# Kernel optimization log

Hardware: AMD Instinct MI355X
Metric: run time of the kernel (lower is better)

The kernel has to match this reference:

```python
import jax, jax.numpy as jnp
import numpy as np

N_IN, N_HID, HEADS = 7, 28, 7
HEAD_DIM = N_HID // HEADS  # 4
LN_EPS = 1e-5


def setup_inputs() -> dict:
    key = jax.random.key(0)
    ks = jax.random.split(key, 16)
    B, S = 16, 1024
    s_in = 1.0 / np.sqrt(N_IN)
    s_hid = 1.0 / np.sqrt(N_HID)
    inp = {
        "inputs": jax.random.normal(ks[0], (B, S, N_IN), dtype=jnp.float32),
        "Wq": jax.random.normal(ks[1], (N_IN, N_HID), dtype=jnp.float32) * s_in,
        "bq": jax.random.normal(ks[2], (N_HID,), dtype=jnp.float32) * s_in,
        "Wk": jax.random.normal(ks[3], (N_IN, N_HID), dtype=jnp.float32) * s_in,
        "bk": jax.random.normal(ks[4], (N_HID,), dtype=jnp.float32) * s_in,
        "Wv": jax.random.normal(ks[5], (N_IN, N_HID), dtype=jnp.float32) * s_in,
        "bv": jax.random.normal(ks[6], (N_HID,), dtype=jnp.float32) * s_in,
        "ln_w": jnp.ones((N_HID,), dtype=jnp.float32),
        "ln_b": jnp.zeros((N_HID,), dtype=jnp.float32),
        "W1": jax.random.normal(ks[7], (N_HID, N_IN), dtype=jnp.float32) * s_hid,
        "b1": jax.random.normal(ks[8], (N_IN,), dtype=jnp.float32) * s_hid,
        "Wq2": jax.random.normal(ks[9], (N_IN, N_HID), dtype=jnp.float32) * s_in,
        "bq2": jax.random.normal(ks[10], (N_HID,), dtype=jnp.float32) * s_in,
        "Wk2": jax.random.normal(ks[11], (N_IN, N_HID), dtype=jnp.float32) * s_in,
        "bk2": jax.random.normal(ks[12], (N_HID,), dtype=jnp.float32) * s_in,
    }
    return inp


def reference(inputs, Wq, bq, Wk, bk, Wv, bv, ln_w, ln_b, W1, b1, Wq2, bq2, Wk2, bk2):
    B, S, _ = inputs.shape
    # QKV projections -> [B, S, H, Dh]
    Q = (inputs @ Wq + bq).reshape(B, S, HEADS, HEAD_DIM)
    K = (inputs @ Wk + bk).reshape(B, S, HEADS, HEAD_DIM)
    V = (inputs @ Wv + bv).reshape(B, S, HEADS, HEAD_DIM)
    # multi-head attention, scores [B, H, Sq, Sk]
    scores = jnp.einsum("bqhd,bkhd->bhqk", Q, K) / jnp.sqrt(jnp.float32(HEAD_DIM))
    attn = jax.nn.softmax(scores, axis=-1)
    out = jnp.einsum("bhqk,bkhd->bqhd", attn, V).reshape(B, S, N_HID)
    # LayerNorm over last dim
    mu = jnp.mean(out, axis=-1, keepdims=True)
    var = jnp.var(out, axis=-1, keepdims=True)
    out = (out - mu) / jnp.sqrt(var + LN_EPS) * ln_w + ln_b
    # FFN + relu + residual
    out = jax.nn.relu(out @ W1 + b1) + inputs  # [B, S, N_IN]
    # second attention (weights only)
    Q2 = out @ Wq2 + bq2  # [B, S, N_HID]
    K2 = out @ Wk2 + bk2
    scores2 = jnp.einsum("bqh,bkh->bqk", Q2, K2) / jnp.sqrt(jnp.float32(N_IN))
    attn2 = jax.nn.softmax(scores2, axis=-1)  # [B, S, S]
    return (out, attn2)
```

## Files before the change

kernel.cpp:

```cpp
#include <hip/hip_runtime.h>

#define BB 16
#define SS 1024
#define NIN 7
#define NHID 28
#define NH 7
#define DH 4

#define EXP2F(x) __builtin_amdgcn_exp2f(x)

constexpr int ROWS = BB * SS;
constexpr int QKV_ELEMS = BB * NH * SS * DH;
constexpr int CHUNK_STRIDE = BB * NH * SS;

__global__ __launch_bounds__(256) void k_proj(
    const float* __restrict__ inp,
    const float* __restrict__ Wq, const float* __restrict__ bq,
    const float* __restrict__ Wk, const float* __restrict__ bk,
    const float* __restrict__ Wv, const float* __restrict__ bv,
    float* __restrict__ Qo, float* __restrict__ Ko, float* __restrict__ Vo)
{
    __shared__ float  xs[256 * NIN];
    __shared__ float4 w4[147];
    __shared__ float4 b4[21];

    const int tid  = threadIdx.x;
    const int row0 = blockIdx.x * 256;

    #pragma unroll
    for (int i = 0; i < NIN; ++i) xs[tid + 256 * i] = inp[row0 * NIN + tid + 256 * i];

    if (tid < 147) {
        const float* src = (tid < 49) ? Wq : (tid < 98) ? Wk : Wv;
        int off = (tid < 49) ? tid : (tid < 98) ? tid - 49 : tid - 98;
        w4[tid] = ((const float4*)src)[off];
    } else if (tid < 168) {
        int t = tid - 147;
        const float* src = (t < 7) ? bq : (t < 14) ? bk : bv;
        b4[t] = ((const float4*)src)[t % 7];
    }
    __syncthreads();

    const int r = row0 + tid;
    const int b = r >> 10, s = r & 1023;

    float x[NIN];
    #pragma unroll
    for (int i = 0; i < NIN; ++i) x[i] = xs[tid * NIN + i];

    float4 q[NH], k[NH], v[NH];
    #pragma unroll
    for (int j4 = 0; j4 < NH; ++j4) { q[j4] = b4[j4]; k[j4] = b4[7 + j4]; v[j4] = b4[14 + j4]; }

    #pragma unroll
    for (int i = 0; i < NIN; ++i) {
        const float xi = x[i];
        #pragma unroll
        for (int j4 = 0; j4 < NH; ++j4) {
            float4 wq = w4[i * 7 + j4];
            float4 wk = w4[49 + i * 7 + j4];
            float4 wv = w4[98 + i * 7 + j4];
            q[j4].x += xi * wq.x; q[j4].y += xi * wq.y; q[j4].z += xi * wq.z; q[j4].w += xi * wq.w;
            k[j4].x += xi * wk.x; k[j4].y += xi * wk.y; k[j4].z += xi * wk.z; k[j4].w += xi * wk.w;
            v[j4].x += xi * wv.x; v[j4].y += xi * wv.y; v[j4].z += xi * wv.z; v[j4].w += xi * wv.w;
        }
    }

    const float qs_scale = 0.5f * 1.4426950408889634f;
    #pragma unroll
    for (int j4 = 0; j4 < NH; ++j4) {
        const int idx = (b * NH + j4) * SS + s;
        float4 qs = make_float4(qs_scale * q[j4].x, qs_scale * q[j4].y,
                                qs_scale * q[j4].z, qs_scale * q[j4].w);
        ((float4*)Qo)[idx] = qs;
        ((float4*)Ko)[idx] = k[j4];
        ((float4*)Vo)[idx] = v[j4];
    }
}

__global__ __launch_bounds__(512) void k_attn1(
    const float* __restrict__ Qo, const float* __restrict__ Ko,
    const float* __restrict__ Vo, float4* __restrict__ Apart,
    float* __restrict__ Lpart)
{
    __shared__ char smem[40960];
    float4* Ksh  = (float4*)smem;
    float4* Vsh  = (float4*)(smem + 4096);
    float4* pacc = (float4*)smem;
    float*  pl   = (float*)(smem + 32768);

    const int bh  = blockIdx.x >> 4;
    const int qt  = (blockIdx.x >> 2) & 3;
    const int ks  = blockIdx.x & 3;
    const int tid = threadIdx.x;

    const float4* Kg = (const float4*)Ko + (size_t)bh * SS + (ks << 8);
    const float4* Vg = (const float4*)Vo + (size_t)bh * SS + (ks << 8);
    if (tid < 256) Ksh[tid]       = Kg[tid];
    else           Vsh[tid - 256] = Vg[tid - 256];

    const int ql = tid & 63;
    const int kq = tid >> 6;

    float4 qv[4];
    #pragma unroll
    for (int r = 0; r < 4; ++r)
        qv[r] = ((const float4*)Qo)[(size_t)bh * SS + (qt << 8) + r * 64 + ql];

    __syncthreads();

    float4 acc[4];
    float  l[4];
    #pragma unroll
    for (int r = 0; r < 4; ++r) { acc[r] = make_float4(0.f, 0.f, 0.f, 0.f); l[r] = 0.f; }

    const int k0 = kq << 5;
    #pragma unroll 4
    for (int kk = k0; kk < k0 + 32; ++kk) {
        float4 kr = Ksh[kk];
        float4 vr = Vsh[kk];
        #pragma unroll
        for (int r = 0; r < 4; ++r) {
            float s = qv[r].x * kr.x + qv[r].y * kr.y + qv[r].z * kr.z + qv[r].w * kr.w;
            float p = EXP2F(s);
            l[r] += p;
            acc[r].x += p * vr.x; acc[r].y += p * vr.y;
            acc[r].z += p * vr.z; acc[r].w += p * vr.w;
        }
    }

    __syncthreads();
    #pragma unroll
    for (int r = 0; r < 4; ++r) {
        pacc[kq * 256 + r * 64 + ql] = acc[r];
        pl[kq * 256 + r * 64 + ql]   = l[r];
    }
    __syncthreads();

    if (tid < 256) {
        float4 a  = pacc[tid];
        float  ll = pl[tid];
        #pragma unroll
        for (int j = 1; j < 8; ++j) {
            float4 t = pacc[j * 256 + tid];
            a.x += t.x; a.y += t.y; a.z += t.z; a.w += t.w;
            ll += pl[j * 256 + tid];
        }
        const size_t o = ((size_t)(ks * (BB * NH) + bh) << 10) + (qt << 8) + tid;
        Apart[o] = a;
        Lpart[o] = ll;
    }
}

__global__ __launch_bounds__(256) void k_lnffn(
    const float4* __restrict__ Apart, const float* __restrict__ Lpart,
    const float* __restrict__ inp,
    const float* __restrict__ lnw, const float* __restrict__ lnb,
    const float* __restrict__ W1, const float* __restrict__ b1,
    const float* __restrict__ Wq2, const float* __restrict__ bq2,
    const float* __restrict__ Wk2, const float* __restrict__ bk2,
    float* __restrict__ outp, float* __restrict__ Q2, float* __restrict__ K2T)
{
    const int r = blockIdx.x * 256 + threadIdx.x;
    const int b = r >> 10, s = r & 1023;

    float y[NHID];
    float mu = 0.f;
    #pragma unroll
    for (int h = 0; h < NH; ++h) {
        const size_t base = ((size_t)(b * NH + h) << 10) + s;
        float4 a  = Apart[base];
        float  ll = Lpart[base];
        #pragma unroll
        for (int c = 1; c < 4; ++c) {
            float4 t = Apart[base + (size_t)c * CHUNK_STRIDE];
            a.x += t.x; a.y += t.y; a.z += t.z; a.w += t.w;
            ll += Lpart[base + (size_t)c * CHUNK_STRIDE];
        }
        const float inv = 1.f / ll;
        y[4 * h + 0] = a.x * inv; y[4 * h + 1] = a.y * inv;
        y[4 * h + 2] = a.z * inv; y[4 * h + 3] = a.w * inv;
        mu += (a.x + a.y + a.z + a.w) * inv;
    }
    mu *= (1.f / NHID);
    float var = 0.f;
    #pragma unroll
    for (int j = 0; j < NHID; ++j) { float d = y[j] - mu; var += d * d; }
    var *= (1.f / NHID);
    const float rstd = rsqrtf(var + 1e-5f);
    #pragma unroll
    for (int j = 0; j < NHID; ++j) y[j] = (y[j] - mu) * rstd * lnw[j] + lnb[j];

    float o[NIN];
    #pragma unroll
    for (int i = 0; i < NIN; ++i) {
        float a = b1[i];
        #pragma unroll
        for (int j = 0; j < NHID; ++j) a += y[j] * W1[j * NIN + i];
        o[i] = fmaxf(a, 0.f) + inp[r * NIN + i];
        outp[r * NIN + i] = o[i];
    }

    const float rs7l2e = 0.3779644730092272f * 1.4426950408889634f;
    float* K2Tb = K2T + ((size_t)b * NHID) * SS + s;
    float4* Q2r = (float4*)Q2 + (size_t)r * 7;
    #pragma unroll
    for (int j4 = 0; j4 < 7; ++j4) {
        float qq[4];
        #pragma unroll
        for (int c = 0; c < 4; ++c) {
            int j = 4 * j4 + c;
            float aq = bq2[j], ak = bk2[j];
            #pragma unroll
            for (int i = 0; i < NIN; ++i) {
                aq += o[i] * Wq2[i * NHID + j];
                ak += o[i] * Wk2[i * NHID + j];
            }
            qq[c] = aq * rs7l2e;
            K2Tb[(size_t)j * SS] = ak;
        }
        Q2r[j4] = make_float4(qq[0], qq[1], qq[2], qq[3]);
    }
}

#define QR 4
__global__ __launch_bounds__(256, 4) void k_attn2(
    const float* __restrict__ Q2, const float* __restrict__ K2T,
    float* __restrict__ out2)
{
    __shared__ float q2s[16 * NHID];

    const int tid  = threadIdx.x;
    const int lane = tid & 63;
    const int wid  = tid >> 6;
    const int row0 = blockIdx.x * 16;
    const int b    = row0 >> 10;

    if (tid < 112) ((float4*)q2s)[tid] = ((const float4*)Q2)[(size_t)row0 * 7 + tid];
    __syncthreads();

    const float*  qw  = q2s + wid * QR * NHID;
    const float4* K2b = (const float4*)(K2T + (size_t)b * NHID * SS);

    float4 p0[QR], p1[QR], p2[QR], p3[QR];
    #pragma unroll
    for (int r = 0; r < QR; ++r) {
        p0[r] = make_float4(0.f, 0.f, 0.f, 0.f);
        p1[r] = make_float4(0.f, 0.f, 0.f, 0.f);
        p2[r] = make_float4(0.f, 0.f, 0.f, 0.f);
        p3[r] = make_float4(0.f, 0.f, 0.f, 0.f);
    }

    #pragma unroll 2
    for (int d = 0; d < NHID; ++d) {
        float4 kt0 = K2b[d * 256 +       lane];
        float4 kt1 = K2b[d * 256 +  64 + lane];
        float4 kt2 = K2b[d * 256 + 128 + lane];
        float4 kt3 = K2b[d * 256 + 192 + lane];
        #pragma unroll
        for (int r = 0; r < QR; ++r) {
            const float qd = qw[r * NHID + d];
            p0[r].x += qd * kt0.x; p0[r].y += qd * kt0.y;
            p0[r].z += qd * kt0.z; p0[r].w += qd * kt0.w;
            p1[r].x += qd * kt1.x; p1[r].y += qd * kt1.y;
            p1[r].z += qd * kt1.z; p1[r].w += qd * kt1.w;
            p2[r].x += qd * kt2.x; p2[r].y += qd * kt2.y;
            p2[r].z += qd * kt2.z; p2[r].w += qd * kt2.w;
            p3[r].x += qd * kt3.x; p3[r].y += qd * kt3.y;
            p3[r].z += qd * kt3.z; p3[r].w += qd * kt3.w;
        }
    }

    #pragma unroll
    for (int r = 0; r < QR; ++r) {
        p0[r].x = EXP2F(p0[r].x); p0[r].y = EXP2F(p0[r].y);
        p0[r].z = EXP2F(p0[r].z); p0[r].w = EXP2F(p0[r].w);
        p1[r].x = EXP2F(p1[r].x); p1[r].y = EXP2F(p1[r].y);
        p1[r].z = EXP2F(p1[r].z); p1[r].w = EXP2F(p1[r].w);
        p2[r].x = EXP2F(p2[r].x); p2[r].y = EXP2F(p2[r].y);
        p2[r].z = EXP2F(p2[r].z); p2[r].w = EXP2F(p2[r].w);
        p3[r].x = EXP2F(p3[r].x); p3[r].y = EXP2F(p3[r].y);
        p3[r].z = EXP2F(p3[r].z); p3[r].w = EXP2F(p3[r].w);
        float sum = p0[r].x + p0[r].y + p0[r].z + p0[r].w
                  + p1[r].x + p1[r].y + p1[r].z + p1[r].w
                  + p2[r].x + p2[r].y + p2[r].z + p2[r].w
                  + p3[r].x + p3[r].y + p3[r].z + p3[r].w;
        #pragma unroll
        for (int off = 1; off < 64; off <<= 1) sum += __shfl_xor(sum, off);
        const float iv = 1.f / sum;
        float4* orow = (float4*)(out2 + ((size_t)row0 + wid * QR + r) * SS);
        orow[       lane] = make_float4(p0[r].x * iv, p0[r].y * iv, p0[r].z * iv, p0[r].w * iv);
        orow[ 64 + lane] = make_float4(p1[r].x * iv, p1[r].y * iv, p1[r].z * iv, p1[r].w * iv);
        orow[128 + lane] = make_float4(p2[r].x * iv, p2[r].y * iv, p2[r].z * iv, p2[r].w * iv);
        orow[192 + lane] = make_float4(p3[r].x * iv, p3[r].y * iv, p3[r].z * iv, p3[r].w * iv);
    }
}

extern "C" void kernel_launch(void* const* d_in, const int* in_sizes, int n_in,
                              void* d_out, int out_size, void* d_ws, size_t ws_size,
                              hipStream_t stream) {
    const float* inp = (const float*)d_in[0];
    const float* Wq  = (const float*)d_in[1];
    const float* bq  = (const float*)d_in[2];
    const float* Wk  = (const float*)d_in[3];
    const float* bk  = (const float*)d_in[4];
    const float* Wv  = (const float*)d_in[5];
    const float* bv  = (const float*)d_in[6];
    const float* lnw = (const float*)d_in[7];
    const float* lnb = (const float*)d_in[8];
    const float* W1  = (const float*)d_in[9];
    const float* b1  = (const float*)d_in[10];
    const float* Wq2 = (const float*)d_in[11];
    const float* bq2 = (const float*)d_in[12];
    const float* Wk2 = (const float*)d_in[13];
    const float* bk2 = (const float*)d_in[14];

    float* out0 = (float*)d_out;
    float* out2 = out0 + ROWS * NIN;

    float4* Apart = (float4*)out2;
    float*  Lpart = out2 + (size_t)4 * QKV_ELEMS;

    float* ws = (float*)d_ws;
    float* Qo  = ws;
    float* Ko  = ws + (size_t)QKV_ELEMS;
    float* Vo  = ws + (size_t)2 * QKV_ELEMS;
    float* Q2  = ws + (size_t)3 * QKV_ELEMS;
    float* K2T = ws + (size_t)4 * QKV_ELEMS;

    k_proj <<<ROWS / 256, 256, 0, stream>>>(inp, Wq, bq, Wk, bk, Wv, bv, Qo, Ko, Vo);
    k_attn1<<<BB * NH * 16, 512, 0, stream>>>(Qo, Ko, Vo, Apart, Lpart);
    k_lnffn<<<ROWS / 256, 256, 0, stream>>>(Apart, Lpart, inp, lnw, lnb, W1, b1,
                                            Wq2, bq2, Wk2, bk2, out0, Q2, K2T);
    k_attn2<<<ROWS / 16, 256, 0, stream>>>(Q2, K2T, out2);
}
```

Baseline: 175.6 us.

## Fuse QKV projection into first attention kernel, computing per-head Q/K/V on the fly

Removes the separate projection kernel and its Q/K/V workspace round trip through global memory. Each attention block now loads raw input rows and the per-head weight slices into shared memory, then computes its query vectors and its key/value tile directly. This saves one launch and the write and reread of the projected tensors. In exchange the projection work is recomputed redundantly across query and key tiles, and the block uses more shared memory.

```diff
diff --git a/kernel.cpp b/kernel.cpp
--- a/kernel.cpp
+++ b/kernel.cpp
@@ -13,79 +13,19 @@
 constexpr int QKV_ELEMS = BB * NH * SS * DH;
 constexpr int CHUNK_STRIDE = BB * NH * SS;
 
-__global__ __launch_bounds__(256) void k_proj(
+__global__ __launch_bounds__(512) void k_attn1(
     const float* __restrict__ inp,
     const float* __restrict__ Wq, const float* __restrict__ bq,
     const float* __restrict__ Wk, const float* __restrict__ bk,
     const float* __restrict__ Wv, const float* __restrict__ bv,
-    float* __restrict__ Qo, float* __restrict__ Ko, float* __restrict__ Vo)
-{
-    __shared__ float  xs[256 * NIN];
-    __shared__ float4 w4[147];
-    __shared__ float4 b4[21];
-
-    const int tid  = threadIdx.x;
-    const int row0 = blockIdx.x * 256;
-
-    #pragma unroll
-    for (int i = 0; i < NIN; ++i) xs[tid + 256 * i] = inp[row0 * NIN + tid + 256 * i];
-
-    if (tid < 147) {
-        const float* src = (tid < 49) ? Wq : (tid < 98) ? Wk : Wv;
-        int off = (tid < 49) ? tid : (tid < 98) ? tid - 49 : tid - 98;
-        w4[tid] = ((const float4*)src)[off];
-    } else if (tid < 168) {
-        int t = tid - 147;
-        const float* src = (t < 7) ? bq : (t < 14) ? bk : bv;
-        b4[t] = ((const float4*)src)[t % 7];
-    }
-    __syncthreads();
-
-    const int r = row0 + tid;
-    const int b = r >> 10, s = r & 1023;
-
-    float x[NIN];
-    #pragma unroll
-    for (int i = 0; i < NIN; ++i) x[i] = xs[tid * NIN + i];
-
-    float4 q[NH], k[NH], v[NH];
-    #pragma unroll
-    for (int j4 = 0; j4 < NH; ++j4) { q[j4] = b4[j4]; k[j4] = b4[7 + j4]; v[j4] = b4[14 + j4]; }
-
-    #pragma unroll
-    for (int i = 0; i < NIN; ++i) {
-        const float xi = x[i];
-        #pragma unroll
-        for (int j4 = 0; j4 < NH; ++j4) {
-            float4 wq = w4[i * 7 + j4];
-            float4 wk = w4[49 + i * 7 + j4];
-            float4 wv = w4[98 + i * 7 + j4];
-            q[j4].x += xi * wq.x; q[j4].y += xi * wq.y; q[j4].z += xi * wq.z; q[j4].w += xi * wq.w;
-            k[j4].x += xi * wk.x; k[j4].y += xi * wk.y; k[j4].z += xi * wk.z; k[j4].w += xi * wk.w;
-            v[j4].x += xi * wv.x; v[j4].y += xi * wv.y; v[j4].z += xi * wv.z; v[j4].w += xi * wv.w;
-        }
-    }
-
-    const float qs_scale = 0.5f * 1.4426950408889634f;
-    #pragma unroll
-    for (int j4 = 0; j4 < NH; ++j4) {
-        const int idx = (b * NH + j4) * SS + s;
-        float4 qs = make_float4(qs_scale * q[j4].x, qs_scale * q[j4].y,
-                                qs_scale * q[j4].z, qs_scale * q[j4].w);
-        ((float4*)Qo)[idx] = qs;
-        ((float4*)Ko)[idx] = k[j4];
-        ((float4*)Vo)[idx] = v[j4];
-    }
-}
-
-__global__ __launch_bounds__(512) void k_attn1(
-    const float* __restrict__ Qo, const float* __restrict__ Ko,
-    const float* __restrict__ Vo, float4* __restrict__ Apart,
-    float* __restrict__ Lpart)
+    float4* __restrict__ Apart, float* __restrict__ Lpart)
 {
     __shared__ char smem[40960];
-    float4* Ksh  = (float4*)smem;
-    float4* Vsh  = (float4*)(smem + 4096);
+    float4* Ksh = (float4*)smem;
+    float4* Vsh = (float4*)(smem + 4096);
+    float*  xq  = (float*)(smem + 8192);
+    float*  xk  = (float*)(smem + 15360);
+    float4* wg  = (float4*)(smem + 22528);
     float4* pacc = (float4*)smem;
     float*  pl   = (float*)(smem + 32768);
 
@@ -93,20 +33,60 @@
     const int qt  = (blockIdx.x >> 2) & 3;
     const int ks  = blockIdx.x & 3;
     const int tid = threadIdx.x;
-
-    const float4* Kg = (const float4*)Ko + (size_t)bh * SS + (ks << 8);
-    const float4* Vg = (const float4*)Vo + (size_t)bh * SS + (ks << 8);
-    if (tid < 256) Ksh[tid]       = Kg[tid];
-    else           Vsh[tid - 256] = Vg[tid - 256];
+    const int b   = bh / NH, h = bh % NH;
+
+    {
+        const float4* xqg = (const float4*)(inp + (size_t)(b * SS + (qt << 8)) * NIN);
+        const float4* xkg = (const float4*)(inp + (size_t)(b * SS + (ks << 8)) * NIN);
+        if (tid < 448) {
+            ((float4*)xq)[tid] = xqg[tid];
+            ((float4*)xk)[tid] = xkg[tid];
+        } else {
+            const int t = tid - 448;
+            if (t < 7)       wg[t] = ((const float4*)Wq)[t * NH + h];
+            else if (t < 14) wg[t] = ((const float4*)Wk)[(t - 7) * NH + h];
+            else if (t < 21) wg[t] = ((const float4*)Wv)[(t - 14) * NH + h];
+            else if (t == 21) wg[21] = ((const float4*)bq)[h];
+            else if (t == 22) wg[22] = ((const float4*)bk)[h];
+            else if (t == 23) wg[23] = ((const float4*)bv)[h];
+        }
+    }
+    __syncthreads();
 
     const int ql = tid & 63;
     const int kq = tid >> 6;
 
+    const float qs_scale = 0.5f * 1.4426950408889634f;
     float4 qv[4];
     #pragma unroll
-    for (int r = 0; r < 4; ++r)
-        qv[r] = ((const float4*)Qo)[(size_t)bh * SS + (qt << 8) + r * 64 + ql];
-
+    for (int r = 0; r < 4; ++r) {
+        float4 a = wg[21];
+        const float* xr = xq + (r * 64 + ql) * NIN;
+        #pragma unroll
+        for (int i = 0; i < NIN; ++i) {
+            const float xi = xr[i];
+            const float4 w = wg[i];
+            a.x += xi * w.x; a.y += xi * w.y; a.z += xi * w.z; a.w += xi * w.w;
+        }
+        qv[r] = make_float4(a.x * qs_scale, a.y * qs_scale,
+                            a.z * qs_scale, a.w * qs_scale);
+    }
+
+    {
+        const int half = tid >> 8;
+        const int key  = tid & 255;
+        const float* xr = xk + key * NIN;
+        const float4* wcol = wg + 7 + half * 7;
+        float4 a = wg[22 + half];
+        #pragma unroll
+        for (int i = 0; i < NIN; ++i) {
+            const float xi = xr[i];
+            const float4 w = wcol[i];
+            a.x += xi * w.x; a.y += xi * w.y; a.z += xi * w.z; a.w += xi * w.w;
+        }
+        if (half == 0) Ksh[key] = a;
+        else           Vsh[key] = a;
+    }
     __syncthreads();
 
     float4 acc[4];
@@ -322,14 +302,11 @@
     float*  Lpart = out2 + (size_t)4 * QKV_ELEMS;
 
     float* ws = (float*)d_ws;
-    float* Qo  = ws;
-    float* Ko  = ws + (size_t)QKV_ELEMS;
-    float* Vo  = ws + (size_t)2 * QKV_ELEMS;
-    float* Q2  = ws + (size_t)3 * QKV_ELEMS;
-    float* K2T = ws + (size_t)4 * QKV_ELEMS;
-
-    k_proj <<<ROWS / 256, 256, 0, stream>>>(inp, Wq, bq, Wk, bk, Wv, bv, Qo, Ko, Vo);
-    k_attn1<<<BB * NH * 16, 512, 0, stream>>>(Qo, Ko, Vo, Apart, Lpart);
+    float* Q2  = ws;
+    float* K2T = ws + (size_t)QKV_ELEMS;
+
+    k_attn1<<<BB * NH * 16, 512, 0, stream>>>(inp, Wq, bq, Wk, bk, Wv, bv,
+                                              Apart, Lpart);
     k_lnffn<<<ROWS / 256, 256, 0, stream>>>(Apart, Lpart, inp, lnw, lnb, W1, b1,
                                             Wq2, bq2, Wk2, bk2, out0, Q2, K2T);
     k_attn2<<<ROWS / 16, 256, 0, stream>>>(Q2, K2T, out2);
```

Result: no change. 174.5 us (-0.6%).
